# Kernel optimization log

Measured on AMD Instinct MI355X. Metric: run time of the kernel, lower is better.

## Reference

```python
import jax, jax.numpy as jnp
import numpy as np

BLOCK_SIZE = 1024
OUTLIER_SIGMA = 3.0
OUT_FEATURES = 11008
IN_FEATURES = 4096
TOKENS = 64


def _quantize_mixed_np(W):
    """Faithful numpy port of quantize_mixed (BLOCK_SIZE divides numel exactly here)."""
    flat = W.astype(np.float32).reshape(-1)
    nb = flat.size // BLOCK_SIZE
    blocks = flat.reshape(nb, BLOCK_SIZE)
    mu = blocks.mean(axis=1, keepdims=True)
    sig = np.maximum(blocks.std(axis=1, ddof=1, keepdims=True), 1e-8)  # torch.std is unbiased
    outlier = np.abs(blocks - mu) > OUTLIER_SIGMA * sig
    abs_max = np.maximum(np.abs(np.where(outlier, 0.0, blocks)).max(axis=1), 1e-8)
    scales = (abs_max / 127.0).astype(np.float16)
    q = np.clip(np.round(blocks / abs_max[:, None] * 127.0), -127, 127).astype(np.int8)
    all_pos = np.arange(nb, dtype=np.int64)[:, None] * BLOCK_SIZE + np.arange(BLOCK_SIZE, dtype=np.int64)[None, :]
    int8_data = q[~outlier]                      # row-major == torch order
    fp16_data = blocks[outlier].astype(np.float16)
    int8_pos = all_pos[~outlier].astype(np.int32)
    fp16_pos = all_pos[outlier].astype(np.int32)
    block_idx = np.nonzero(~outlier)[0].astype(np.int32)  # block index per int8 value
    return int8_data, fp16_data, scales, int8_pos, fp16_pos, block_idx


def setup_inputs() -> dict:
    key = jax.random.key(0)
    k_x, k_b = jax.random.split(key)
    rng = np.random.default_rng(0)
    W = (rng.standard_normal((OUT_FEATURES, IN_FEATURES)) * 0.02).astype(np.float32)
    int8_data, fp16_data, scales, int8_pos, fp16_pos, block_idx = _quantize_mixed_np(W)
    x = jax.random.normal(k_x, (TOKENS, IN_FEATURES), dtype=jnp.float16)
    bias = jax.random.normal(k_b, (OUT_FEATURES,), dtype=jnp.float16) * jnp.float16(0.02)
    return {
        "x": x,
        "int8_data": jnp.asarray(int8_data),
        "fp16_data": jnp.asarray(fp16_data),
        "scales": jnp.asarray(scales),
        "bias": bias,
        "int8_pos": jnp.asarray(int8_pos),
        "fp16_pos": jnp.asarray(fp16_pos),
        "block_idx": jnp.asarray(block_idx),
    }


def reference(x, int8_data, fp16_data, scales, bias, int8_pos, fp16_pos, block_idx):
    out_features = bias.shape[0]
    in_features = x.shape[1]
    numel = out_features * in_features  # divisible by BLOCK_SIZE for these dims
    # dequantize_mixed: scatter fp16 outliers and dequantized int8 values into flat fp16 buffer
    flat = jnp.zeros((numel,), dtype=jnp.float16)
    flat = flat.at[fp16_pos].set(fp16_data)
    flat = flat.at[int8_pos].set(int8_data.astype(jnp.float16) * scales[block_idx])
    W = flat.reshape(out_features, in_features)
    # F.linear(x, W, bias) in fp16
    return jnp.dot(x.astype(jnp.float16), W.T) + bias
```

## Files before the change

kernel.cpp:

```cpp
#include <hip/hip_runtime.h>
#include <hip/hip_fp16.h>

#define TOK   64
#define INF   4096
#define OUTF  11008
#define NUMEL (OUTF * INF)
#define NSLC  (NUMEL / 64)
#define NBLK  (OUTF / 16)
#define KSPL  8

typedef __attribute__((ext_vector_type(8))) _Float16 half8;
typedef __attribute__((ext_vector_type(4))) _Float16 half4;
typedef __attribute__((ext_vector_type(4))) float floatx4;
typedef __attribute__((ext_vector_type(4), aligned(4))) int int4u;

#define BPAD 520

__global__ __launch_bounds__(256) void precompute_kernel(
    const float* __restrict__ x, const int* __restrict__ fppos, int nf,
    _Float16* __restrict__ x16, int* __restrict__ cum64) {
  const int t = blockIdx.x * 256 + threadIdx.x;
  if (t < (TOK * INF) / 4) {
    const floatx4 f = *(const floatx4*)&x[t * 4];
    half4 h;
    h[0] = (_Float16)f[0]; h[1] = (_Float16)f[1];
    h[2] = (_Float16)f[2]; h[3] = (_Float16)f[3];
    *(half4*)&x16[t * 4] = h;
  }
  if (t <= NSLC) {
    const int target = t << 6;
    int lo = 0, hi = nf;
    while (lo < hi) {
      const int mid = (lo + hi) >> 1;
      if (fppos[mid] < target) lo = mid + 1; else hi = mid;
    }
    cum64[t] = lo;
  }
}

__device__ __forceinline__ half8 dq_slot(
    const int p0, const float s,
    const int* __restrict__ i8, const float* __restrict__ fpdat,
    const int* __restrict__ fppos, const int* __restrict__ cum64,
    const int n8) {
  const int s64 = p0 >> 6;
  const int c0  = cum64[s64];
  const int c1  = cum64[s64 + 1];

  int lt = 0, f = 0;
  float ov[8];
#pragma unroll
  for (int e = 0; e < 8; ++e) ov[e] = 0.f;

  const int w = c1 - c0;
  if (w > 0) {
    {
      const int d = fppos[c0] - p0;
      const float v = fpdat[c0];
      lt += (d < 0);
      if ((unsigned)d < 8u) {
        f |= 1 << d;
#pragma unroll
        for (int e = 0; e < 8; ++e) ov[e] = (d == e) ? v : ov[e];
      }
    }
    if (w > 1) {
      const int d = fppos[c0 + 1] - p0;
      const float v = fpdat[c0 + 1];
      lt += (d < 0);
      if ((unsigned)d < 8u) {
        f |= 1 << d;
#pragma unroll
        for (int e = 0; e < 8; ++e) ov[e] = (d == e) ? v : ov[e];
      }
    }
    for (int j = 2; j < w; ++j) {
      const int d = fppos[c0 + j] - p0;
      const float v = fpdat[c0 + j];
      lt += (d < 0);
      if ((unsigned)d < 8u) {
        f |= 1 << d;
#pragma unroll
        for (int e = 0; e < 8; ++e) ov[e] = (d == e) ? v : ov[e];
      }
    }
  }

  const int i0 = p0 - c0 - lt;
  half8 oh;
  if (i0 + 8 <= n8) {
    int l[8];
    *(int4u*)&l[0] = *(const int4u*)&i8[i0];
    *(int4u*)&l[4] = *(const int4u*)&i8[i0 + 4];
    if (f == 0) {
#pragma unroll
      for (int e = 0; e < 8; ++e) oh[e] = (_Float16)((float)l[e] * s);
    } else {
      int q = 0;
#pragma unroll
      for (int e = 0; e < 8; ++e) {
        const int flg = (f >> e) & 1;
        int lv = l[0];
#pragma unroll
        for (int qq = 1; qq < 8; ++qq) lv = (q == qq) ? l[qq] : lv;
        oh[e] = flg ? (_Float16)ov[e] : (_Float16)((float)lv * s);
        q += 1 - flg;
      }
    }
  } else {
    int c = 0;
    const int m = n8 - 1;
#pragma unroll
    for (int e = 0; e < 8; ++e) {
      const int flg = (f >> e) & 1;
      int idx = i0 + e - c;
      idx = idx < 0 ? 0 : (idx > m ? m : idx);
      oh[e] = flg ? (_Float16)ov[e] : (_Float16)((float)i8[idx] * s);
      c += flg;
    }
  }
  return oh;
}

__global__ __launch_bounds__(256) void gemm_fused(
    const _Float16* __restrict__ x16,
    const int* __restrict__ i8, const float* __restrict__ fpdat,
    const int* __restrict__ fppos, const float* __restrict__ scales,
    const int* __restrict__ cum64, const float* __restrict__ bias,
    float* __restrict__ out, const int n8) {
  __shared__ __attribute__((aligned(16))) char smem[16 * BPAD * 2];
  _Float16 (* __restrict__ Bt)[BPAD] = (_Float16 (*)[BPAD])smem;
  float* red = (float*)smem;

  const int tid  = threadIdx.x;
  const int wave = tid >> 6;
  const int lane = tid & 63;
  const int quad = lane >> 4;
  const int ln   = lane & 15;
  const int nt   = blockIdx.x >> 3;
  const int kq   = blockIdx.x & 7;
  const int n0   = nt * 16;
  const int kbas = kq * 512;

#pragma unroll 2
  for (int i = 0; i < 4; ++i) {
    const int slot = i * 256 + tid;
    const int r    = slot >> 6;
    const int k8   = slot & 63;
    const int p0   = (n0 + r) * INF + kbas + k8 * 8;
    const float s  = scales[p0 >> 10];
    const half8 oh = dq_slot(p0, s, i8, fpdat, fppos, cum64, n8);
    *(half8*)&Bt[r][k8 * 8] = oh;
  }
  __syncthreads();

  const int ko0 = wave * 128 + quad * 8;
  const _Float16* ap = &x16[ln * INF + kbas + ko0];
  const _Float16* bp = &Bt[ln][ko0];

  floatx4 acc0 = {0,0,0,0}, acc1 = {0,0,0,0}, acc2 = {0,0,0,0}, acc3 = {0,0,0,0};
#pragma unroll
  for (int st = 0; st < 4; ++st) {
    const int ko = st * 32;
    const half8 bh = *(const half8*)&bp[ko];
    const half8 a0 = *(const half8*)&ap[ko];
    const half8 a1 = *(const half8*)&ap[16 * INF + ko];
    const half8 a2 = *(const half8*)&ap[32 * INF + ko];
    const half8 a3 = *(const half8*)&ap[48 * INF + ko];
    acc0 = __builtin_amdgcn_mfma_f32_16x16x32_f16(a0, bh, acc0, 0, 0, 0);
    acc1 = __builtin_amdgcn_mfma_f32_16x16x32_f16(a1, bh, acc1, 0, 0, 0);
    acc2 = __builtin_amdgcn_mfma_f32_16x16x32_f16(a2, bh, acc2, 0, 0, 0);
    acc3 = __builtin_amdgcn_mfma_f32_16x16x32_f16(a3, bh, acc3, 0, 0, 0);
  }
  __syncthreads();

  const int mb = quad * 4;
#pragma unroll
  for (int i = 0; i < 4; ++i) red[wave * 1024 + (mb + i)      * 16 + ln] = acc0[i];
#pragma unroll
  for (int i = 0; i < 4; ++i) red[wave * 1024 + (16 + mb + i) * 16 + ln] = acc1[i];
#pragma unroll
  for (int i = 0; i < 4; ++i) red[wave * 1024 + (32 + mb + i) * 16 + ln] = acc2[i];
#pragma unroll
  for (int i = 0; i < 4; ++i) red[wave * 1024 + (48 + mb + i) * 16 + ln] = acc3[i];
  __syncthreads();

#pragma unroll
  for (int c2 = 0; c2 < 4; ++c2) {
    const int cell = tid + c2 * 256;
    const int mm = cell >> 4, nn = cell & 15;
    float v = red[cell] + red[1024 + cell] + red[2048 + cell] + red[3072 + cell];
    if (kq == 0) v += bias[n0 + nn];
    atomicAdd(&out[mm * OUTF + n0 + nn], v);
  }
}

extern "C" void kernel_launch(void* const* d_in, const int* in_sizes, int n_in,
                              void* d_out, int out_size, void* d_ws,
                              size_t ws_size, hipStream_t stream) {
  const float* x      = (const float*)d_in[0];
  const int*   i8     = (const int*)d_in[1];
  const float* fpdat  = (const float*)d_in[2];
  const float* scales = (const float*)d_in[3];
  const float* bias   = (const float*)d_in[4];
  const int*   fppos  = (const int*)d_in[6];

  char* wsp = (char*)d_ws;
  _Float16* x16   = (_Float16*)wsp;
  int*      cum64 = (int*)(wsp + (size_t)TOK * INF * sizeof(_Float16));
  float*    out   = (float*)d_out;

  const int n8 = in_sizes[1];
  const int nf = in_sizes[2];

  hipMemsetAsync(out, 0, (size_t)out_size * sizeof(float), stream);
  precompute_kernel<<<(NSLC + 256) / 256 + 1, 256, 0, stream>>>(x, fppos, nf,
                                                                x16, cum64);
  gemm_fused<<<NBLK * KSPL, 256, 0, stream>>>(x16, i8, fpdat, fppos, scales,
                                              cum64, bias, out, n8);
}
```

Measured before the change: 452.3 us.

## Precompute per-64-slice outlier bitmasks and replace atomics with split-K reduce kernel

The precompute kernel now stores, for each 64-element slice, the outlier prefix count and a 64-bit outlier bitmask. The GEMM dequant step uses popcount on that mask instead of scanning fppos entries per slot, and loads all slot metadata up front. The atomicAdd split-K accumulation and the memset are replaced by per-split partial buffers plus a separate reduce kernel that adds the bias. The trade-off is more workspace, about 22 MB of partial-sum traffic and an extra launch, in exchange for no atomics and less divergent scanning.

New measurement: 446.0 us. No clear change (-1.4%).

```diff
diff --git a/kernel.cpp b/kernel.cpp
--- a/kernel.cpp
+++ b/kernel.cpp
@@ -8,17 +8,19 @@
 #define NSLC  (NUMEL / 64)
 #define NBLK  (OUTF / 16)
 #define KSPL  8
+#define OUTN  (TOK * OUTF)
 
 typedef __attribute__((ext_vector_type(8))) _Float16 half8;
 typedef __attribute__((ext_vector_type(4))) _Float16 half4;
 typedef __attribute__((ext_vector_type(4))) float floatx4;
 typedef __attribute__((ext_vector_type(4), aligned(4))) int int4u;
+typedef __attribute__((ext_vector_type(4))) int int4a;
 
 #define BPAD 520
 
 __global__ __launch_bounds__(256) void precompute_kernel(
     const float* __restrict__ x, const int* __restrict__ fppos, int nf,
-    _Float16* __restrict__ x16, int* __restrict__ cum64) {
+    _Float16* __restrict__ x16, int* __restrict__ meta) {
   const int t = blockIdx.x * 256 + threadIdx.x;
   if (t < (TOK * INF) / 4) {
     const floatx4 f = *(const floatx4*)&x[t * 4];
@@ -27,66 +29,53 @@
     h[2] = (_Float16)f[2]; h[3] = (_Float16)f[3];
     *(half4*)&x16[t * 4] = h;
   }
-  if (t <= NSLC) {
+  if (t < NSLC) {
     const int target = t << 6;
     int lo = 0, hi = nf;
     while (lo < hi) {
       const int mid = (lo + hi) >> 1;
       if (fppos[mid] < target) lo = mid + 1; else hi = mid;
     }
-    cum64[t] = lo;
-  }
-}
-
-__device__ __forceinline__ half8 dq_slot(
-    const int p0, const float s,
-    const int* __restrict__ i8, const float* __restrict__ fpdat,
-    const int* __restrict__ fppos, const int* __restrict__ cum64,
-    const int n8) {
-  const int s64 = p0 >> 6;
-  const int c0  = cum64[s64];
-  const int c1  = cum64[s64 + 1];
-
-  int lt = 0, f = 0;
+    unsigned long long mask = 0ull;
+    int j = lo;
+    while (j < nf) {
+      const int d = fppos[j] - target;
+      if (d >= 64) break;
+      mask |= 1ull << d;
+      ++j;
+    }
+    int4a mv;
+    mv[0] = lo;
+    mv[1] = (int)(unsigned)(mask & 0xffffffffu);
+    mv[2] = (int)(unsigned)(mask >> 32);
+    mv[3] = 0;
+    *(int4a*)&meta[t * 4] = mv;
+  }
+}
+
+__device__ __forceinline__ half8 dq_slot_meta(
+    const int p0, const int c0, const unsigned mlo, const unsigned mhi,
+    const float s, const int* __restrict__ i8,
+    const float* __restrict__ fpdat, const int n8) {
+  const int off = p0 & 63;
+  const unsigned m8 = 0xffu & (off < 32 ? (mlo >> off) : (mhi >> (off - 32)));
+  const unsigned bl = (off >= 32) ? mlo : (mlo & ((1u << off) - 1u));
+  const unsigned bh = (off >= 32) ? (mhi & ((1u << (off - 32)) - 1u)) : 0u;
+  const int lt = __popc(bl) + __popc(bh);
+  const int i0 = p0 - c0 - lt;
+  const int f  = (int)m8;
+
   float ov[8];
 #pragma unroll
   for (int e = 0; e < 8; ++e) ov[e] = 0.f;
-
-  const int w = c1 - c0;
-  if (w > 0) {
-    {
-      const int d = fppos[c0] - p0;
-      const float v = fpdat[c0];
-      lt += (d < 0);
-      if ((unsigned)d < 8u) {
-        f |= 1 << d;
-#pragma unroll
-        for (int e = 0; e < 8; ++e) ov[e] = (d == e) ? v : ov[e];
-      }
-    }
-    if (w > 1) {
-      const int d = fppos[c0 + 1] - p0;
-      const float v = fpdat[c0 + 1];
-      lt += (d < 0);
-      if ((unsigned)d < 8u) {
-        f |= 1 << d;
-#pragma unroll
-        for (int e = 0; e < 8; ++e) ov[e] = (d == e) ? v : ov[e];
-      }
-    }
-    for (int j = 2; j < w; ++j) {
-      const int d = fppos[c0 + j] - p0;
-      const float v = fpdat[c0 + j];
-      lt += (d < 0);
-      if ((unsigned)d < 8u) {
-        f |= 1 << d;
-#pragma unroll
-        for (int e = 0; e < 8; ++e) ov[e] = (d == e) ? v : ov[e];
-      }
-    }
-  }
-
-  const int i0 = p0 - c0 - lt;
+  if (f) {
+    int fi = c0 + lt;
+#pragma unroll
+    for (int e = 0; e < 8; ++e) {
+      if ((f >> e) & 1) { ov[e] = fpdat[fi]; ++fi; }
+    }
+  }
+
   half8 oh;
   if (i0 + 8 <= n8) {
     int l[8];
@@ -125,9 +114,8 @@
 __global__ __launch_bounds__(256) void gemm_fused(
     const _Float16* __restrict__ x16,
     const int* __restrict__ i8, const float* __restrict__ fpdat,
-    const int* __restrict__ fppos, const float* __restrict__ scales,
-    const int* __restrict__ cum64, const float* __restrict__ bias,
-    float* __restrict__ out, const int n8) {
+    const float* __restrict__ scales, const int* __restrict__ meta,
+    float* __restrict__ part, const int n8) {
   __shared__ __attribute__((aligned(16))) char smem[16 * BPAD * 2];
   _Float16 (* __restrict__ Bt)[BPAD] = (_Float16 (*)[BPAD])smem;
   float* red = (float*)smem;
@@ -142,14 +130,30 @@
   const int n0   = nt * 16;
   const int kbas = kq * 512;
 
-#pragma unroll 2
+  int p0v[4], c0v[4];
+  unsigned mlov[4], mhiv[4];
+  float sv[4];
+#pragma unroll
   for (int i = 0; i < 4; ++i) {
     const int slot = i * 256 + tid;
     const int r    = slot >> 6;
     const int k8   = slot & 63;
     const int p0   = (n0 + r) * INF + kbas + k8 * 8;
-    const float s  = scales[p0 >> 10];
-    const half8 oh = dq_slot(p0, s, i8, fpdat, fppos, cum64, n8);
+    const int4a mv = *(const int4a*)&meta[(p0 >> 6) * 4];
+    p0v[i] = p0;
+    c0v[i] = mv[0];
+    mlov[i] = (unsigned)mv[1];
+    mhiv[i] = (unsigned)mv[2];
+    sv[i]  = scales[p0 >> 10];
+  }
+
+#pragma unroll
+  for (int i = 0; i < 4; ++i) {
+    const int slot = i * 256 + tid;
+    const int r    = slot >> 6;
+    const int k8   = slot & 63;
+    const half8 oh = dq_slot_meta(p0v[i], c0v[i], mlov[i], mhiv[i], sv[i],
+                                  i8, fpdat, n8);
     *(half8*)&Bt[r][k8 * 8] = oh;
   }
   __syncthreads();
@@ -185,14 +189,31 @@
   for (int i = 0; i < 4; ++i) red[wave * 1024 + (48 + mb + i) * 16 + ln] = acc3[i];
   __syncthreads();
 
+  float* pp = &part[(size_t)kq * OUTN];
 #pragma unroll
   for (int c2 = 0; c2 < 4; ++c2) {
     const int cell = tid + c2 * 256;
     const int mm = cell >> 4, nn = cell & 15;
-    float v = red[cell] + red[1024 + cell] + red[2048 + cell] + red[3072 + cell];
-    if (kq == 0) v += bias[n0 + nn];
-    atomicAdd(&out[mm * OUTF + n0 + nn], v);
-  }
+    pp[mm * OUTF + n0 + nn] =
+        red[cell] + red[1024 + cell] + red[2048 + cell] + red[3072 + cell];
+  }
+}
+
+__global__ __launch_bounds__(256) void reduce_kernel(
+    const float* __restrict__ part, const float* __restrict__ bias,
+    float* __restrict__ out) {
+  const int t  = blockIdx.x * 256 + threadIdx.x;
+  const int i4 = t * 4;
+  floatx4 a = *(const floatx4*)&part[i4];
+#pragma unroll
+  for (int k = 1; k < KSPL; ++k) {
+    const floatx4 b = *(const floatx4*)&part[(size_t)k * OUTN + i4];
+    a[0] += b[0]; a[1] += b[1]; a[2] += b[2]; a[3] += b[3];
+  }
+  const int nn = i4 % OUTF;
+  const floatx4 bb = *(const floatx4*)&bias[nn];
+  a[0] += bb[0]; a[1] += bb[1]; a[2] += bb[2]; a[3] += bb[3];
+  *(floatx4*)&out[i4] = a;
 }
 
 extern "C" void kernel_launch(void* const* d_in, const int* in_sizes, int n_in,
@@ -206,16 +227,17 @@
   const int*   fppos  = (const int*)d_in[6];
 
   char* wsp = (char*)d_ws;
-  _Float16* x16   = (_Float16*)wsp;
-  int*      cum64 = (int*)(wsp + (size_t)TOK * INF * sizeof(_Float16));
-  float*    out   = (float*)d_out;
+  _Float16* x16  = (_Float16*)wsp;
+  int*      meta = (int*)(wsp + (size_t)TOK * INF * sizeof(_Float16));
+  float*    part = (float*)(wsp + (size_t)TOK * INF * sizeof(_Float16)
+                                + (size_t)NSLC * 16);
+  float*    out  = (float*)d_out;
 
   const int n8 = in_sizes[1];
   const int nf = in_sizes[2];
 
-  hipMemsetAsync(out, 0, (size_t)out_size * sizeof(float), stream);
-  precompute_kernel<<<(NSLC + 256) / 256 + 1, 256, 0, stream>>>(x, fppos, nf,
-                                                                x16, cum64);
-  gemm_fused<<<NBLK * KSPL, 256, 0, stream>>>(x16, i8, fpdat, fppos, scales,
-                                              cum64, bias, out, n8);
-}
+  precompute_kernel<<<NSLC / 256, 256, 0, stream>>>(x, fppos, nf, x16, meta);
+  gemm_fused<<<NBLK * KSPL, 256, 0, stream>>>(x16, i8, fpdat, scales, meta,
+                                              part, n8);
+  reduce_kernel<<<OUTN / (4 * 256), 256, 0, stream>>>(part, bias, out);
+}
```
